# Optimization experiments

Measured on AMD Instinct MI355X. Metric: run time of the kernel, lower is better.

The kernel has to match this reference:

```python
import jax, jax.numpy as jnp
import numpy as np
import math

H = 768      # hidden_size
NH = 12      # num_attention_heads
HS = H // NH # head_size


def setup_inputs() -> dict:
    key = jax.random.key(0)
    ks = jax.random.split(key, 6)
    B, T = 16, 512
    x = jax.random.normal(ks[0], (B, T, H), dtype=jnp.float32)
    attention_mask = jnp.ones((B, T), dtype=jnp.int64)
    s = 0.02
    W_qkv = jax.random.normal(ks[1], (H, 3 * H), dtype=jnp.float32) * s
    b_qkv = jnp.zeros((3 * H,), dtype=jnp.float32)
    W_proj = jax.random.normal(ks[2], (H, H), dtype=jnp.float32) * s
    b_proj = jnp.zeros((H,), dtype=jnp.float32)
    return {"x": x, "attention_mask": attention_mask, "W_qkv": W_qkv,
            "b_qkv": b_qkv, "W_proj": W_proj, "b_proj": b_proj}


def reference(x, attention_mask, W_qkv, b_qkv, W_proj, b_proj):
    B, T, C = x.shape
    qkv = x @ W_qkv + b_qkv                      # [B,T,3H]
    q, k, v = jnp.split(qkv, 3, axis=2)
    # [B,T,H] -> [B,NH,T,HS]
    q = q.reshape(B, T, NH, HS).transpose(0, 2, 1, 3)
    k = k.reshape(B, T, NH, HS).transpose(0, 2, 1, 3)
    v = v.reshape(B, T, NH, HS).transpose(0, 2, 1, 3)
    att = jnp.einsum('bhqd,bhkd->bhqk', q, k) / math.sqrt(HS)
    mask = attention_mask[:, None, None, :]      # [B,1,1,T]
    neg = jnp.finfo(att.dtype).min
    att = jnp.where(mask == 0, neg, att)
    att = jax.nn.softmax(att, axis=-1)
    # dropout is identity in eval / p=0
    y = jnp.einsum('bhqk,bhkd->bhqd', att, v)    # [B,NH,T,HS]
    y = y.transpose(0, 2, 1, 3).reshape(B, T, C)
    y = y @ W_proj + b_proj
    return y
```

## Files before the change

kernel.cpp:

```cpp
#include <hip/hip_runtime.h>


typedef unsigned short u16;
typedef __bf16 bf16x8 __attribute__((ext_vector_type(8)));
typedef float f32x4 __attribute__((ext_vector_type(4)));
typedef unsigned short u16x8 __attribute__((ext_vector_type(8)));

__device__ __forceinline__ u16 f2b(float f) {
  union { float f; unsigned int u; } v; v.f = f;
  unsigned int u = v.u;
  return (u16)((u + 0x7FFFu + ((u >> 16) & 1u)) >> 16);
}

__device__ __forceinline__ void gload_lds16(const u16* gsrc, u16* ldst) {
  __builtin_amdgcn_global_load_lds(
      (const __attribute__((address_space(1))) void*)gsrc,
      (__attribute__((address_space(3))) void*)ldst,
      16, 0, 0);
}

__device__ __forceinline__ bf16x8 lds_read16(const u16* p) {
  return __builtin_bit_cast(bf16x8, *(const int4*)p);
}


__global__ __launch_bounds__(256) void cvt_x(const float* __restrict__ in,
                                             u16* __restrict__ out, int n8) {
  int i = blockIdx.x * 256 + threadIdx.x;
  if (i >= n8) return;
  float4 v0 = ((const float4*)in)[(size_t)i * 2];
  float4 v1 = ((const float4*)in)[(size_t)i * 2 + 1];
  u16x8 r;
  r[0] = f2b(v0.x); r[1] = f2b(v0.y); r[2] = f2b(v0.z); r[3] = f2b(v0.w);
  r[4] = f2b(v1.x); r[5] = f2b(v1.y); r[6] = f2b(v1.z); r[7] = f2b(v1.w);
  *(u16x8*)(out + (size_t)i * 8) = r;
}

__global__ __launch_bounds__(256) void transpose_cvt(const float* __restrict__ in,
                                                     u16* __restrict__ out, int R, int C) {
  __shared__ float tile[32][33];
  int nbx = C >> 5;
  int bx = blockIdx.x % nbx, by = blockIdx.x / nbx;
  int tx = threadIdx.x & 31, ty = threadIdx.x >> 5;
#pragma unroll
  for (int jj = 0; jj < 32; jj += 8)
    tile[ty + jj][tx] = in[(size_t)(by * 32 + ty + jj) * C + bx * 32 + tx];
  __syncthreads();
#pragma unroll
  for (int jj = 0; jj < 32; jj += 8)
    out[(size_t)(bx * 32 + ty + jj) * R + by * 32 + tx] = f2b(tile[tx][ty + jj]);
}


__global__ __launch_bounds__(256) void gemm_qkv(const u16* __restrict__ A,
                                                const u16* __restrict__ Bt,
                                                const float* __restrict__ bias,
                                                u16* __restrict__ qk,
                                                u16* __restrict__ vt) {
  constexpr int K = 768, KT = 12, NBX = 18;
  __shared__ __align__(16) u16 As[2][128 * 64];
  __shared__ __align__(16) u16 Bs[2][128 * 64];
  const int t = threadIdx.x, l = t & 63, w = t >> 6;
  const int wr = w >> 1, wc = w & 1;
  const int lm = l & 15, g = l >> 4;
  const int cpx = gridDim.x >> 3;
  const int bid = (blockIdx.x & 7) * cpx + (blockIdx.x >> 3);
  const int brow = (bid / NBX) << 7;
  const int bcol = (bid % NBX) << 7;

  f32x4 acc[4][4] = {};

  const int rs = t >> 3, cs = t & 7;
  const int swz = (cs ^ (rs & 7)) * 8;
  const u16* gA = A + (size_t)(brow + rs) * K + swz;
  const u16* gB = Bt + (size_t)(bcol + rs) * K + swz;

  auto stage = [&](int kt, int buf) {
    const int k0 = kt << 6;
#pragma unroll
    for (int p = 0; p < 4; ++p)
      gload_lds16(gA + (size_t)p * 32 * K + k0, As[buf] + p * 2048 + t * 8);
#pragma unroll
    for (int p = 0; p < 4; ++p)
      gload_lds16(gB + (size_t)p * 32 * K + k0, Bs[buf] + p * 2048 + t * 8);
  };

  stage(0, 0);
  __syncthreads();

  for (int kt = 0; kt < KT; ++kt) {
    const int cur = kt & 1;
    if (kt + 1 < KT) stage(kt + 1, cur ^ 1);
    bf16x8 af[4][2], bf_[4][2];
#pragma unroll
    for (int m = 0; m < 4; ++m) {
      int r = wr * 64 + m * 16 + lm;
#pragma unroll
      for (int ks = 0; ks < 2; ++ks)
        af[m][ks] = lds_read16(As[cur] + r * 64 + (((ks * 4 + g) ^ (r & 7)) * 8));
    }
#pragma unroll
    for (int n = 0; n < 4; ++n) {
      int r = wc * 64 + n * 16 + lm;
#pragma unroll
      for (int ks = 0; ks < 2; ++ks)
        bf_[n][ks] = lds_read16(Bs[cur] + r * 64 + (((ks * 4 + g) ^ (r & 7)) * 8));
    }
    __builtin_amdgcn_s_setprio(1);
#pragma unroll
    for (int m = 0; m < 4; ++m)
#pragma unroll
      for (int n = 0; n < 4; ++n)
#pragma unroll
        for (int ks = 0; ks < 2; ++ks)
          acc[m][n] = __builtin_amdgcn_mfma_f32_16x16x32_bf16(af[m][ks], bf_[n][ks],
                                                              acc[m][n], 0, 0, 0);
    __builtin_amdgcn_s_setprio(0);
    __syncthreads();
  }

  if (bcol >= 1536) {
    const int b = brow >> 9;
#pragma unroll
    for (int n = 0; n < 4; ++n) {
      int cv = bcol - 1536 + wc * 64 + n * 16 + lm;
      int hh = cv >> 6, dd = cv & 63;
      float bv = bias[1536 + cv];
      u16* vrow = vt + (((size_t)(b * 12 + hh) * 64 + dd) << 9);
#pragma unroll
      for (int m = 0; m < 4; ++m) {
        int tq = (brow + wr * 64 + m * 16 + g * 4) & 511;
        ushort4 pk;
        pk.x = f2b(acc[m][n][0] + bv);
        pk.y = f2b(acc[m][n][1] + bv);
        pk.z = f2b(acc[m][n][2] + bv);
        pk.w = f2b(acc[m][n][3] + bv);
        *(ushort4*)(vrow + tq) = pk;
      }
    }
  } else {
#pragma unroll
    for (int n = 0; n < 4; ++n) {
      int c = bcol + wc * 64 + n * 16 + lm;
      float bv = bias[c];
#pragma unroll
      for (int m = 0; m < 4; ++m) {
        int rbase = brow + wr * 64 + m * 16 + g * 4;
#pragma unroll
        for (int j = 0; j < 4; ++j)
          qk[(size_t)(rbase + j) * 1536 + c] = f2b(acc[m][n][j] + bv);
      }
    }
  }
}

__global__ __launch_bounds__(256) void gemm_proj(const u16* __restrict__ A,
                                                 const u16* __restrict__ Bt,
                                                 const float* __restrict__ bias,
                                                 float* __restrict__ out) {
  constexpr int K = 768, KT = 12, NBX = 6, N = 768;
  __shared__ __align__(16) u16 As[2][128 * 64];
  __shared__ __align__(16) u16 Bs[2][128 * 64];
  const int t = threadIdx.x, l = t & 63, w = t >> 6;
  const int wr = w >> 1, wc = w & 1;
  const int lm = l & 15, g = l >> 4;
  const int cpx = gridDim.x >> 3;
  const int bid = (blockIdx.x & 7) * cpx + (blockIdx.x >> 3);
  const int brow = (bid / NBX) << 7;
  const int bcol = (bid % NBX) << 7;

  f32x4 acc[4][4] = {};

  const int rs = t >> 3, cs = t & 7;
  const int swz = (cs ^ (rs & 7)) * 8;
  const u16* gA = A + (size_t)(brow + rs) * K + swz;
  const u16* gB = Bt + (size_t)(bcol + rs) * K + swz;

  auto stage = [&](int kt, int buf) {
    const int k0 = kt << 6;
#pragma unroll
    for (int p = 0; p < 4; ++p)
      gload_lds16(gA + (size_t)p * 32 * K + k0, As[buf] + p * 2048 + t * 8);
#pragma unroll
    for (int p = 0; p < 4; ++p)
      gload_lds16(gB + (size_t)p * 32 * K + k0, Bs[buf] + p * 2048 + t * 8);
  };

  stage(0, 0);
  __syncthreads();

  for (int kt = 0; kt < KT; ++kt) {
    const int cur = kt & 1;
    if (kt + 1 < KT) stage(kt + 1, cur ^ 1);
    bf16x8 af[4][2], bf_[4][2];
#pragma unroll
    for (int m = 0; m < 4; ++m) {
      int r = wr * 64 + m * 16 + lm;
#pragma unroll
      for (int ks = 0; ks < 2; ++ks)
        af[m][ks] = lds_read16(As[cur] + r * 64 + (((ks * 4 + g) ^ (r & 7)) * 8));
    }
#pragma unroll
    for (int n = 0; n < 4; ++n) {
      int r = wc * 64 + n * 16 + lm;
#pragma unroll
      for (int ks = 0; ks < 2; ++ks)
        bf_[n][ks] = lds_read16(Bs[cur] + r * 64 + (((ks * 4 + g) ^ (r & 7)) * 8));
    }
    __builtin_amdgcn_s_setprio(1);
#pragma unroll
    for (int m = 0; m < 4; ++m)
#pragma unroll
      for (int n = 0; n < 4; ++n)
#pragma unroll
        for (int ks = 0; ks < 2; ++ks)
          acc[m][n] = __builtin_amdgcn_mfma_f32_16x16x32_bf16(af[m][ks], bf_[n][ks],
                                                              acc[m][n], 0, 0, 0);
    __builtin_amdgcn_s_setprio(0);
    __syncthreads();
  }

#pragma unroll
  for (int n = 0; n < 4; ++n) {
    int c = bcol + wc * 64 + n * 16 + lm;
    float bv = bias[c];
#pragma unroll
    for (int m = 0; m < 4; ++m) {
      int rbase = brow + wr * 64 + m * 16 + g * 4;
#pragma unroll
      for (int j = 0; j < 4; ++j)
        out[(size_t)(rbase + j) * N + c] = acc[m][n][j] + bv;
    }
  }
}


__global__ __launch_bounds__(256) void attn_fused(const u16* __restrict__ qk,
                                                  const u16* __restrict__ vt,
                                                  const int* __restrict__ mask,
                                                  u16* __restrict__ out) {
  __shared__ __align__(16) u16 Ks[2][64 * 64];
  __shared__ __align__(16) u16 Vs[2][64 * 64];
  __shared__ __align__(16) u16 Ps[4][16 * 64];

  const int t = threadIdx.x, l = t & 63, w = t >> 6;
  const int lm = l & 15, g = l >> 4;
  const int bid = (blockIdx.x & 7) * 192 + (blockIdx.x >> 3);
  const int qt = bid & 7;
  const int bh = bid >> 3;
  const int b = bh / 12, h = bh % 12;

  bf16x8 qf[2];
  {
    const u16* qptr = qk + (size_t)(b * 512 + qt * 64 + w * 16 + lm) * 1536 + h * 64;
    qf[0] = *(const bf16x8*)(qptr + g * 8);
    qf[1] = *(const bf16x8*)(qptr + 32 + g * 8);
  }

  unsigned mbits = 0;
#pragma unroll
  for (int kt = 0; kt < 8; ++kt)
#pragma unroll
    for (int n = 0; n < 4; ++n)
      mbits |= (mask[b * 512 + kt * 64 + n * 16 + lm] != 0 ? 1u : 0u) << (kt * 4 + n);

  bf16x8 ones;
  {
    u16x8 o1;
#pragma unroll
    for (int e = 0; e < 8; ++e) o1[e] = 0x3F80;
    ones = __builtin_bit_cast(bf16x8, o1);
  }

  f32x4 o[4] = {};
  f32x4 osum = {};

  const int rk = t >> 3, ck = t & 7;
  const int cswz = ck ^ (rk & 7);
  const u16* srcK = qk + (size_t)(b * 512 + rk) * 1536 + 768 + h * 64 + cswz * 8;
  const u16* srcV = vt + ((size_t)(bh * 64 + rk)) * 512 + cswz * 8;

  auto stage = [&](int kt, int buf) {
    const size_t offK = (size_t)kt * 64 * 1536;
    gload_lds16(srcK + offK, Ks[buf] + t * 8);
    gload_lds16(srcK + offK + 32 * 1536, Ks[buf] + (t + 256) * 8);
    gload_lds16(srcV + kt * 64, Vs[buf] + t * 8);
    gload_lds16(srcV + kt * 64 + 32 * 512, Vs[buf] + (t + 256) * 8);
  };

  stage(0, 0);
  __syncthreads();
  int cur = 0;

  for (int kt = 0; kt < 8; ++kt) {
    if (kt < 7) stage(kt + 1, cur ^ 1);

    f32x4 s[4] = {};
#pragma unroll
    for (int ds = 0; ds < 2; ++ds) {
#pragma unroll
      for (int n = 0; n < 4; ++n) {
        int r = n * 16 + lm;
        bf16x8 kf = lds_read16(Ks[cur] + r * 64 + (((ds * 4 + g) ^ (r & 7)) * 8));
        s[n] = __builtin_amdgcn_mfma_f32_16x16x32_bf16(qf[ds], kf, s[n], 0, 0, 0);
      }
    }
    u16* pw = Ps[w];
#pragma unroll
    for (int n = 0; n < 4; ++n) {
      bool ok = (mbits >> (kt * 4 + n)) & 1u;
      int key = n * 16 + lm;
#pragma unroll
      for (int j = 0; j < 4; ++j) {
        float sv = ok ? s[n][j] * 0.125f : -3.0e38f;
        float p = __expf(sv);
        int q16 = g * 4 + j;
        pw[q16 * 64 + (((key >> 3) ^ (q16 & 7)) * 8) + (key & 7)] = f2b(p);
      }
    }
#pragma unroll
    for (int ks = 0; ks < 2; ++ks) {
      bf16x8 pa = lds_read16(pw + lm * 64 + (((ks * 4 + g) ^ (lm & 7)) * 8));
#pragma unroll
      for (int n = 0; n < 4; ++n) {
        int rd = n * 16 + lm;
        bf16x8 vb = lds_read16(Vs[cur] + rd * 64 + (((ks * 4 + g) ^ (rd & 7)) * 8));
        o[n] = __builtin_amdgcn_mfma_f32_16x16x32_bf16(pa, vb, o[n], 0, 0, 0);
      }
      osum = __builtin_amdgcn_mfma_f32_16x16x32_bf16(pa, ones, osum, 0, 0, 0);
    }
    __syncthreads();
    cur ^= 1;
  }

  float inv[4];
#pragma unroll
  for (int j = 0; j < 4; ++j) inv[j] = 1.0f / osum[j];
#pragma unroll
  for (int n = 0; n < 4; ++n) {
    int d = n * 16 + lm;
#pragma unroll
    for (int j = 0; j < 4; ++j) {
      int tq = qt * 64 + w * 16 + g * 4 + j;
      out[(size_t)(b * 512 + tq) * 768 + h * 64 + d] = f2b(o[n][j] * inv[j]);
    }
  }
}


extern "C" void kernel_launch(void* const* d_in, const int* in_sizes, int n_in,
                              void* d_out, int out_size, void* d_ws, size_t ws_size,
                              hipStream_t stream) {
  const float* x = (const float*)d_in[0];
  const int* mask = (const int*)d_in[1];
  const float* Wqkv = (const float*)d_in[2];
  const float* bqkv = (const float*)d_in[3];
  const float* Wproj = (const float*)d_in[4];
  const float* bproj = (const float*)d_in[5];
  float* out = (float*)d_out;

  char* ws = (char*)d_ws;
  u16* xb     = (u16*)(ws);
  u16* wqkvT  = (u16*)(ws + 12582912);
  u16* wprojT = (u16*)(ws + 16121856);
  u16* qkb    = (u16*)(ws + 17301504);
  u16* vtb    = (u16*)(ws + 42467328);
  u16* attnb  = (u16*)(ws + 55050240);

  cvt_x<<<3072, 256, 0, stream>>>(x, xb, 786432);
  transpose_cvt<<<72 * 24, 256, 0, stream>>>(Wqkv, wqkvT, 768, 2304);
  transpose_cvt<<<24 * 24, 256, 0, stream>>>(Wproj, wprojT, 768, 768);
  gemm_qkv<<<1152, 256, 0, stream>>>(xb, wqkvT, bqkv, qkb, vtb);
  attn_fused<<<1536, 256, 0, stream>>>(qkb, vtb, mask, attnb);
  gemm_proj<<<384, 256, 0, stream>>>(attnb, wprojT, bproj, out);
}
```

Before: 105.3 us.

## Load QKV GEMM fragments directly from global into registers, dropping LDS staging

The QKV projection GEMM no longer stages A and B tiles through double-buffered LDS with async global-to-LDS loads and barriers. Each wave now loads its MFMA fragments straight from global memory into two register sets and alternates between them across k-steps, with no __syncthreads. Launch bounds are set to 2 blocks per SM. This removes LDS traffic and barriers, but tiles shared between waves are now fetched separately by each wave. The global reads are also 16-byte accesses strided by row, which depends on L2/L1 hits and raises register pressure.

Measured after the change: 175.6 us. 66.8% more time.

```diff
diff --git a/kernel.cpp b/kernel.cpp
--- a/kernel.cpp
+++ b/kernel.cpp
@@ -52,14 +52,12 @@
 }
 
 
-__global__ __launch_bounds__(256) void gemm_qkv(const u16* __restrict__ A,
-                                                const u16* __restrict__ Bt,
-                                                const float* __restrict__ bias,
-                                                u16* __restrict__ qk,
-                                                u16* __restrict__ vt) {
-  constexpr int K = 768, KT = 12, NBX = 18;
-  __shared__ __align__(16) u16 As[2][128 * 64];
-  __shared__ __align__(16) u16 Bs[2][128 * 64];
+__global__ __launch_bounds__(256, 2) void gemm_qkv(const u16* __restrict__ A,
+                                                   const u16* __restrict__ Bt,
+                                                   const float* __restrict__ bias,
+                                                   u16* __restrict__ qk,
+                                                   u16* __restrict__ vt) {
+  constexpr int K = 768, NBX = 18;
   const int t = threadIdx.x, l = t & 63, w = t >> 6;
   const int wr = w >> 1, wc = w & 1;
   const int lm = l & 15, g = l >> 4;
@@ -70,42 +68,21 @@
 
   f32x4 acc[4][4] = {};
 
-  const int rs = t >> 3, cs = t & 7;
-  const int swz = (cs ^ (rs & 7)) * 8;
-  const u16* gA = A + (size_t)(brow + rs) * K + swz;
-  const u16* gB = Bt + (size_t)(bcol + rs) * K + swz;
-
-  auto stage = [&](int kt, int buf) {
-    const int k0 = kt << 6;
-#pragma unroll
-    for (int p = 0; p < 4; ++p)
-      gload_lds16(gA + (size_t)p * 32 * K + k0, As[buf] + p * 2048 + t * 8);
-#pragma unroll
-    for (int p = 0; p < 4; ++p)
-      gload_lds16(gB + (size_t)p * 32 * K + k0, Bs[buf] + p * 2048 + t * 8);
+  const u16* pa = A + (size_t)(brow + wr * 64 + lm) * K + g * 8;
+  const u16* pb = Bt + (size_t)(bcol + wc * 64 + lm) * K + g * 8;
+
+  bf16x8 aA[4][2], bA[4][2], aB[4][2], bB[4][2];
+
+  auto loadf = [&](int kt, bf16x8 af[4][2], bf16x8 bf[4][2]) {
+#pragma unroll
+    for (int m = 0; m < 4; ++m)
+#pragma unroll
+      for (int ks = 0; ks < 2; ++ks) {
+        af[m][ks] = *(const bf16x8*)(pa + (size_t)(m * 16) * K + kt * 64 + ks * 32);
+        bf[m][ks] = *(const bf16x8*)(pb + (size_t)(m * 16) * K + kt * 64 + ks * 32);
+      }
   };
-
-  stage(0, 0);
-  __syncthreads();
-
-  for (int kt = 0; kt < KT; ++kt) {
-    const int cur = kt & 1;
-    if (kt + 1 < KT) stage(kt + 1, cur ^ 1);
-    bf16x8 af[4][2], bf_[4][2];
-#pragma unroll
-    for (int m = 0; m < 4; ++m) {
-      int r = wr * 64 + m * 16 + lm;
-#pragma unroll
-      for (int ks = 0; ks < 2; ++ks)
-        af[m][ks] = lds_read16(As[cur] + r * 64 + (((ks * 4 + g) ^ (r & 7)) * 8));
-    }
-#pragma unroll
-    for (int n = 0; n < 4; ++n) {
-      int r = wc * 64 + n * 16 + lm;
-#pragma unroll
-      for (int ks = 0; ks < 2; ++ks)
-        bf_[n][ks] = lds_read16(Bs[cur] + r * 64 + (((ks * 4 + g) ^ (r & 7)) * 8));
-    }
+  auto mm = [&](bf16x8 af[4][2], bf16x8 bf[4][2]) {
     __builtin_amdgcn_s_setprio(1);
 #pragma unroll
     for (int m = 0; m < 4; ++m)
@@ -113,10 +90,18 @@
       for (int n = 0; n < 4; ++n)
 #pragma unroll
         for (int ks = 0; ks < 2; ++ks)
-          acc[m][n] = __builtin_amdgcn_mfma_f32_16x16x32_bf16(af[m][ks], bf_[n][ks],
+          acc[m][n] = __builtin_amdgcn_mfma_f32_16x16x32_bf16(af[m][ks], bf[n][ks],
                                                               acc[m][n], 0, 0, 0);
     __builtin_amdgcn_s_setprio(0);
-    __syncthreads();
+  };
+
+  loadf(0, aA, bA);
+#pragma unroll
+  for (int kt = 0; kt < 12; kt += 2) {
+    loadf(kt + 1, aB, bB);
+    mm(aA, bA);
+    if (kt + 2 < 12) loadf(kt + 2, aA, bA);
+    mm(aB, bB);
   }
 
   if (bcol >= 1536) {
@@ -234,7 +219,6 @@
   }
 }
 
-
 __global__ __launch_bounds__(256) void attn_fused(const u16* __restrict__ qk,
                                                   const u16* __restrict__ vt,
                                                   const int* __restrict__ mask,
```
